# Kernel tuning notes

Measured on AMD Instinct MI355X. Metric: run time of the kernel, lower is better.

Reference implementation:

```python
import jax, jax.numpy as jnp
import numpy as np

B, L, N, HID, NH, HD, SH, SW, MH = 1, 512, 2048, 2048, 16, 128, 64, 32, 8192


def _rms(x, w, eps=1e-6):
    return x * jax.lax.rsqrt(jnp.mean(x * x, axis=-1, keepdims=True) + eps) * w


def _adaln(x, emb, W, b, nw):
    e = jax.nn.silu(emb) @ W + b  # [B, 6*hid]
    sh_m, sc_m, g_m, sh_p, sc_p, g_p = jnp.split(e, 6, axis=-1)
    xm = _rms(x, nw) * (1.0 + sc_m[:, None]) + sh_m[:, None]
    return xm, g_m, sh_p, sc_p, g_p


def _rope(x, rope):
    # x: [B, H, S, D], rope: [S, 1, D]
    f = rope[:, 0]  # [S, D]
    cos = jnp.repeat(f[:, 0::2], 2, axis=-1)[None, None]
    sin = jnp.repeat(f[:, 1::2], 2, axis=-1)[None, None]
    xr = x.reshape(*x.shape[:-1], -1, 2)
    x_rot = jnp.stack([-xr[..., 1], xr[..., 0]], axis=-1).reshape(x.shape)
    return x * cos + x_rot * sin


def _sdpa(q, k, v, scale):
    s = jnp.einsum('bhqd,bhkd->bhqk', q, k) * scale
    return jnp.einsum('bhqk,bhkd->bhqd', jax.nn.softmax(s, axis=-1), v)


def _mlp(x, w1, b1, w2, b2):
    return jax.nn.gelu(x @ w1 + b1, approximate=True) @ w2 + b2


def setup_inputs() -> dict:
    key = jax.random.key(0)
    ks = iter(jax.random.split(key, 32))
    r = lambda *s: jax.random.normal(next(ks), s, dtype=jnp.float32) * 0.02
    inp = {
        'txt': jax.random.normal(next(ks), (B, L, HID), dtype=jnp.float32),
        'img': jax.random.normal(next(ks), (B, N, HID), dtype=jnp.float32),
        'vec': jax.random.normal(next(ks), (B, HID), dtype=jnp.float32),
        'rope': jax.random.normal(next(ks), (N, 1, HD), dtype=jnp.float32),
        'sol_temperature': jax.random.uniform(next(ks), (B, 64), dtype=jnp.float32),
        'sol_spatial': jax.random.normal(next(ks), (B, 8, 8), dtype=jnp.float32),
        'ada_img_w': r(HID, 6 * HID), 'ada_img_b': jnp.zeros(6 * HID, jnp.float32), 'ada_img_nw': jnp.ones(HID, jnp.float32),
        'ada_txt_w': r(HID, 6 * HID), 'ada_txt_b': jnp.zeros(6 * HID, jnp.float32), 'ada_txt_nw': jnp.ones(HID, jnp.float32),
        'txt_qkv_w': r(HID, 3 * HID), 'img_qkv_w': r(HID, 3 * HID),
        'txt_out_w': r(HID, HID), 'img_out_w': r(HID, HID),
        'mod_w': r(NH) * 5.0, 'mod_b': r(NH) * 5.0,
        'img_n2_w': jnp.ones(HID, jnp.float32), 'txt_n2_w': jnp.ones(HID, jnp.float32),
        'img_fc1_w': r(HID, MH), 'img_fc1_b': jnp.zeros(MH, jnp.float32),
        'img_fc2_w': r(MH, HID), 'img_fc2_b': jnp.zeros(HID, jnp.float32),
        'txt_fc1_w': r(HID, MH), 'txt_fc1_b': jnp.zeros(MH, jnp.float32),
        'txt_fc2_w': r(MH, HID), 'txt_fc2_b': jnp.zeros(HID, jnp.float32),
        'spatial_h': SH, 'spatial_w': SW,
    }
    return inp


def reference(txt, img, vec, rope, sol_temperature, sol_spatial,
              ada_img_w, ada_img_b, ada_img_nw, ada_txt_w, ada_txt_b, ada_txt_nw,
              txt_qkv_w, img_qkv_w, txt_out_w, img_out_w, mod_w, mod_b,
              img_n2_w, txt_n2_w, img_fc1_w, img_fc1_b, img_fc2_w, img_fc2_b,
              txt_fc1_w, txt_fc1_b, txt_fc2_w, txt_fc2_b, spatial_h, spatial_w):
    b, l, hid = txt.shape
    n = img.shape[1]
    nh = mod_w.shape[0]
    hd = hid // nh
    scale = hd ** (-0.5)

    img_n, img_g, img_shp, img_scp, img_gp = _adaln(img, vec, ada_img_w, ada_img_b, ada_img_nw)
    txt_n, txt_g, txt_shp, txt_scp, txt_gp = _adaln(txt, vec, ada_txt_w, ada_txt_b, ada_txt_nw)

    def qkv(x, w, s):
        p = (x @ w).reshape(b, s, 3, nh, hd).transpose(2, 0, 3, 1, 4)  # [3,B,H,S,D]
        return p[0], p[1], p[2]

    tq, tk, tv = qkv(txt_n, txt_qkv_w, l)
    iq, ik, iv = qkv(img_n, img_qkv_w, n)
    iq = _rope(iq, rope)
    ik = _rope(ik, rope)

    # SOL spatial modulation: bilinear upsample (align_corners=False) + 1x1 conv + exp(clamp)
    sol_up = jax.image.resize(sol_spatial, (b, spatial_h, spatial_w), 'bilinear')
    mod = sol_up[:, None] * mod_w[None, :, None, None] + mod_b[None, :, None, None]
    mod = jnp.exp(jnp.clip(mod, -2.0, 2.0)).reshape(b, nh, n, 1)
    iq = iq * mod
    ik = ik * mod

    k = jnp.concatenate([tk, ik], axis=2)  # [B,H,L+N,D]
    v = jnp.concatenate([tv, iv], axis=2)

    txt_attn = _sdpa(tq, k, v, scale).transpose(0, 2, 1, 3).reshape(b, l, hid) @ txt_out_w

    temp = jnp.clip(jnp.mean(sol_temperature, axis=1, keepdims=True), 0.1)  # [B,1]
    s_eff = jnp.sqrt(scale / temp)[:, :, None, None]  # [B,1,1,1]
    img_attn = _sdpa(iq * s_eff, k * s_eff, v, 1.0).transpose(0, 2, 1, 3).reshape(b, n, hid) @ img_out_w

    txt = txt + txt_g[:, None] * txt_attn
    img = img + img_g[:, None] * img_attn

    txt_in = _rms(txt, txt_n2_w) * (1.0 + txt_scp[:, None]) + txt_shp[:, None]
    img_in = _rms(img, img_n2_w) * (1.0 + img_scp[:, None]) + img_shp[:, None]
    txt = txt + txt_gp[:, None] * _mlp(txt_in, txt_fc1_w, txt_fc1_b, txt_fc2_w, txt_fc2_b)
    img = img + img_gp[:, None] * _mlp(img_in, img_fc1_w, img_fc1_b, img_fc2_w, img_fc2_b)
    return txt, img
```

## Files before the change

### kernel.cpp

```cpp
#include <hip/hip_runtime.h>

typedef short short8 __attribute__((ext_vector_type(8)));
typedef float f32x4 __attribute__((ext_vector_type(4)));

__device__ __forceinline__ unsigned short f2bu(float f) {
  unsigned u = __builtin_bit_cast(unsigned, f);
  u += 0x7fffu + ((u >> 16) & 1u);
  return (unsigned short)(u >> 16);
}

__device__ __forceinline__ unsigned short f2bt(float f) {
  return (unsigned short)(__builtin_bit_cast(unsigned, f) >> 16);
}

__device__ __forceinline__ float b2f(unsigned short b) {
  unsigned u = (unsigned)b << 16;
  return __builtin_bit_cast(float, u);
}

__device__ __forceinline__ float gelu_t(float x) {
  float x3 = x * x * x;
  float t = tanhf(0.7978845608028654f * (x + 0.044715f * x3));
  return 0.5f * x * (1.f + t);
}

__device__ __forceinline__ void gload16(const void* g, void* l) {
  __builtin_amdgcn_global_load_lds(
      (const __attribute__((address_space(1))) void*)g,
      (__attribute__((address_space(3))) void*)l, 16, 0, 0);
}

__global__ __launch_bounds__(256) void prep_small(
    const float* __restrict__ vec, const float* __restrict__ sol_t,
    float* __restrict__ silu_vec, float* __restrict__ scales) {
  __shared__ float red[4];
  int t = threadIdx.x;
  float v = (t < 64) ? sol_t[t] : 0.f;
#pragma unroll
  for (int o = 32; o > 0; o >>= 1) v += __shfl_down(v, o);
  if ((t & 63) == 0) red[t >> 6] = v;
  __syncthreads();
  if (t == 0) {
    float m = (red[0] + red[1] + red[2] + red[3]) * (1.f / 64.f);
    m = fmaxf(m, 0.1f);
    const float sc = 0.08838834764831845f;
    const float l2e = 1.4426950408889634f;
    scales[0] = sc * l2e;
    scales[1] = sc / m * l2e;
  }
  for (int k = t; k < 2048; k += 256) {
    float x = vec[k];
    silu_vec[k] = x / (1.f + expf(-x));
  }
}

__global__ __launch_bounds__(256) void mod_kernel(
    const float* __restrict__ S, const float* __restrict__ mw,
    const float* __restrict__ mb, float* __restrict__ modb) {
  int idx = blockIdx.x * 256 + threadIdx.x;
  int h = idx >> 11, n = idx & 2047;
  int y = n >> 5, x = n & 31;
  float cy = (y + 0.5f) * 0.125f - 0.5f;
  float cx = (x + 0.5f) * 0.25f - 0.5f;
  int y0 = (int)floorf(cy); float fy = cy - (float)y0;
  int x0 = (int)floorf(cx); float fx = cx - (float)x0;
  int y0c = min(max(y0, 0), 7), y1c = min(max(y0 + 1, 0), 7);
  int x0c = min(max(x0, 0), 7), x1c = min(max(x0 + 1, 0), 7);
  float v = (1.f - fy) * ((1.f - fx) * S[y0c * 8 + x0c] + fx * S[y0c * 8 + x1c]) +
            fy * ((1.f - fx) * S[y1c * 8 + x0c] + fx * S[y1c * 8 + x1c]);
  float t = v * mw[h] + mb[h];
  t = fminf(fmaxf(t, -2.f), 2.f);
  modb[idx] = expf(t);
}

__global__ __launch_bounds__(256) void ada_gemv(
    const float* __restrict__ sv,
    const float* __restrict__ Wi, const float* __restrict__ bi,
    const float* __restrict__ Wt, const float* __restrict__ bt,
    float* __restrict__ ei, float* __restrict__ et) {
  __shared__ float red[4][64];
  const float* W = blockIdx.y ? Wt : Wi;
  const float* bb = blockIdx.y ? bt : bi;
  float* e = blockIdx.y ? et : ei;
  int jl = threadIdx.x & 63, ks = threadIdx.x >> 6;
  int j = blockIdx.x * 64 + jl;
  float acc = 0.f;
  int k0 = ks * 512;
#pragma unroll 4
  for (int k = 0; k < 512; ++k) acc += sv[k0 + k] * W[(size_t)(k0 + k) * 12288 + j];
  red[ks][jl] = acc;
  __syncthreads();
  if (ks == 0) e[j] = red[0][jl] + red[1][jl] + red[2][jl] + red[3][jl] + bb[j];
}

__global__ __launch_bounds__(256) void norm1_kernel(
    const float* __restrict__ txt, const float* __restrict__ img,
    const float* __restrict__ nw_t, const float* __restrict__ nw_i,
    const float* __restrict__ e_t, const float* __restrict__ e_i,
    unsigned short* __restrict__ out) {
  __shared__ float red[4];
  int r = blockIdx.x, t = threadIdx.x;
  bool ist = r < 512;
  const float* X = ist ? txt + (size_t)r * 2048 : img + (size_t)(r - 512) * 2048;
  const float* nw = ist ? nw_t : nw_i;
  const float* e = ist ? e_t : e_i;
  const float4* xr = reinterpret_cast<const float4*>(X);
  float4 v0 = xr[t * 2], v1 = xr[t * 2 + 1];
  float ss = v0.x * v0.x + v0.y * v0.y + v0.z * v0.z + v0.w * v0.w +
             v1.x * v1.x + v1.y * v1.y + v1.z * v1.z + v1.w * v1.w;
#pragma unroll
  for (int o = 32; o > 0; o >>= 1) ss += __shfl_down(ss, o);
  if ((t & 63) == 0) red[t >> 6] = ss;
  __syncthreads();
  float rinv = rsqrtf((red[0] + red[1] + red[2] + red[3]) * (1.f / 2048.f) + 1e-6f);
  int c0 = t * 8;
  float xv[8] = {v0.x, v0.y, v0.z, v0.w, v1.x, v1.y, v1.z, v1.w};
  short8 ov;
#pragma unroll
  for (int i = 0; i < 8; ++i) {
    int c = c0 + i;
    float y = xv[i] * rinv * nw[c] * (1.f + e[2048 + c]) + e[c];
    ov[i] = (short)f2bu(y);
  }
  *reinterpret_cast<short8*>(out + (size_t)r * 2048 + c0) = ov;
}

__global__ __launch_bounds__(256) void res1_rms(
    const float* __restrict__ txt, const float* __restrict__ img,
    const float* __restrict__ P0, const float* __restrict__ P1,
    const float* __restrict__ e_t, const float* __restrict__ e_i,
    const float* __restrict__ nw_t, const float* __restrict__ nw_i,
    float* __restrict__ out, unsigned short* __restrict__ actA) {
  __shared__ float red[4];
  int r = blockIdx.x, t = threadIdx.x;
  bool ist = r < 512;
  const float* X = ist ? txt + (size_t)r * 2048 : img + (size_t)(r - 512) * 2048;
  const float* e = ist ? e_t : e_i;
  const float* nw = ist ? nw_t : nw_i;
  int c0 = t * 8;
  const float* p0 = P0 + (size_t)r * 2048 + c0;
  const float* p1 = P1 + (size_t)r * 2048 + c0;
  float o[8];
  float ss = 0.f;
#pragma unroll
  for (int i = 0; i < 8; i += 4) {
    float4 x = *reinterpret_cast<const float4*>(X + c0 + i);
    float4 a = *reinterpret_cast<const float4*>(p0 + i);
    float4 b = *reinterpret_cast<const float4*>(p1 + i);
    float4 g = *reinterpret_cast<const float4*>(e + 4096 + c0 + i);
    o[i + 0] = x.x + g.x * (a.x + b.x);
    o[i + 1] = x.y + g.y * (a.y + b.y);
    o[i + 2] = x.z + g.z * (a.z + b.z);
    o[i + 3] = x.w + g.w * (a.w + b.w);
    ss += o[i] * o[i] + o[i + 1] * o[i + 1] + o[i + 2] * o[i + 2] + o[i + 3] * o[i + 3];
  }
  *reinterpret_cast<float4*>(out + (size_t)r * 2048 + c0) =
      make_float4(o[0], o[1], o[2], o[3]);
  *reinterpret_cast<float4*>(out + (size_t)r * 2048 + c0 + 4) =
      make_float4(o[4], o[5], o[6], o[7]);
#pragma unroll
  for (int of = 32; of > 0; of >>= 1) ss += __shfl_down(ss, of);
  if ((t & 63) == 0) red[t >> 6] = ss;
  __syncthreads();
  float rinv = rsqrtf((red[0] + red[1] + red[2] + red[3]) * (1.f / 2048.f) + 1e-6f);
  short8 ov;
#pragma unroll
  for (int i = 0; i < 8; ++i) {
    int c = c0 + i;
    float y = o[i] * rinv * nw[c] * (1.f + e[8192 + c]) + e[6144 + c];
    ov[i] = (short)f2bu(y);
  }
  *reinterpret_cast<short8*>(actA + (size_t)r * 2048 + c0) = ov;
}

__global__ __launch_bounds__(256) void res2_kernel(
    const float* __restrict__ P0, const float* __restrict__ P1,
    const float* __restrict__ b_t, const float* __restrict__ b_i,
    const float* __restrict__ e_t, const float* __restrict__ e_i,
    float* __restrict__ out) {
  int r = blockIdx.x, t = threadIdx.x;
  bool ist = r < 512;
  const float* e = ist ? e_t : e_i;
  const float* bb = ist ? b_t : b_i;
  int c0 = t * 8;
  const float* p0 = P0 + (size_t)r * 2048 + c0;
  const float* p1 = P1 + (size_t)r * 2048 + c0;
  float* op = out + (size_t)r * 2048 + c0;
#pragma unroll
  for (int i = 0; i < 8; i += 4) {
    float4 a = *reinterpret_cast<const float4*>(p0 + i);
    float4 b = *reinterpret_cast<const float4*>(p1 + i);
    float4 g = *reinterpret_cast<const float4*>(e + 10240 + c0 + i);
    float4 bv = *reinterpret_cast<const float4*>(bb + c0 + i);
    float4 o = *reinterpret_cast<const float4*>(op + i);
    o.x += g.x * (a.x + b.x + bv.x);
    o.y += g.y * (a.y + b.y + bv.y);
    o.z += g.z * (a.z + b.z + bv.z);
    o.w += g.w * (a.w + b.w + bv.w);
    *reinterpret_cast<float4*>(op + i) = o;
  }
}

__global__ __launch_bounds__(256) void transpose_w(
    const float* __restrict__ W, unsigned short* __restrict__ Bt, int K, int N) {
  __shared__ float tile[64][33];
  int n0 = blockIdx.x * 32, k0 = blockIdx.y * 64;
  int tid = threadIdx.x;
  int tx = tid & 31, ty = tid >> 5;
#pragma unroll
  for (int j = 0; j < 8; ++j)
    tile[ty + j * 8][tx] = W[(size_t)(k0 + ty + j * 8) * N + n0 + tx];
  __syncthreads();
  int n = tid >> 3, ks = (tid & 7) * 8;
  unsigned pk[4];
#pragma unroll
  for (int i = 0; i < 4; ++i) {
    float lo = tile[ks + 2 * i][n], hi = tile[ks + 2 * i + 1][n];
    pk[i] = (unsigned)f2bu(lo) | ((unsigned)f2bu(hi) << 16);
  }
  int4 ov = make_int4(pk[0], pk[1], pk[2], pk[3]);
  *reinterpret_cast<int4*>(Bt + (size_t)(n0 + n) * K + k0 + ks) = ov;
}

__global__ __launch_bounds__(256) void transpose_v(
    const unsigned short* __restrict__ V, unsigned short* __restrict__ Vt) {
  __shared__ unsigned short tile[32][33];
  int h = blockIdx.z;
  int s0 = blockIdx.x * 32, d0 = blockIdx.y * 32;
  int tx = threadIdx.x, ty = threadIdx.y;
  const unsigned short* src = V + (size_t)h * 2560 * 128;
  unsigned short* dst = Vt + (size_t)h * 128 * 2560;
#pragma unroll
  for (int j = 0; j < 32; j += 8)
    tile[ty + j][tx] = src[(size_t)(s0 + ty + j) * 128 + d0 + tx];
  __syncthreads();
#pragma unroll
  for (int j = 0; j < 32; j += 8)
    dst[(size_t)(d0 + ty + j) * 2560 + s0 + tx] = tile[tx][ty + j];
}

struct GemmP {
  const unsigned short *A, *Bt_t, *Bt_i;
  float* C;
  unsigned short* Cb;
  const float *bias_t, *bias_i;
  const float *rope, *modb;
  unsigned short *q_txt, *q_img, *k_cat, *v_cat;
  const float* scales;
  int Mb_t;
  int N, K, KS;
};

template <int EPI>
__global__ __launch_bounds__(256) void gemm2(GemmP p) {
  __shared__ __align__(16) char GRAW[65536];
  int4* sAb = reinterpret_cast<int4*>(GRAW);
  int4* sBb = reinterpret_cast<int4*>(GRAW + 32768);
  const int NB = gridDim.x, MBT = gridDim.y;
  int nwg = NB * MBT;
  int orig = blockIdx.y * NB + blockIdx.x;
  int qq = nwg >> 3, rr = nwg & 7, xcd = orig & 7, base = orig >> 3;
  int sw = (xcd < rr ? xcd * (qq + 1) : rr * (qq + 1) + (xcd - rr) * qq) + base;
  int bx = sw / MBT, by = sw % MBT;
  const bool is_t = by < p.Mb_t;
  const unsigned short* Bt = is_t ? p.Bt_t : p.Bt_i;
  const int m0 = by * 128, n0 = bx * 128;
  const int z = blockIdx.z;
  const int Kz = p.K / p.KS, kbeg = z * Kz, kend = kbeg + Kz;
  const int tid = threadIdx.x;
  const int w = tid >> 6, l = tid & 63, lr = l & 15, lg = l >> 4;
  const int wm = (w >> 1) * 64, wn = (w & 1) * 64;
  f32x4 acc[4][4] = {};
  const int4* Ag = reinterpret_cast<const int4*>(p.A);
  const int4* Bg = reinterpret_cast<const int4*>(Bt);
  const int K8 = p.K >> 3;
  int srow[4], sch[4];
#pragma unroll
  for (int i = 0; i < 4; ++i) {
    int s = i * 256 + tid;
    srow[i] = s >> 3;
    sch[i] = (s & 7) ^ (srow[i] & 7);
  }
  {
    int kc = kbeg >> 3;
#pragma unroll
    for (int i = 0; i < 4; ++i) {
      gload16(&Ag[(size_t)(m0 + srow[i]) * K8 + kc + sch[i]], &sAb[i * 256 + w * 64]);
      gload16(&Bg[(size_t)(n0 + srow[i]) * K8 + kc + sch[i]], &sBb[i * 256 + w * 64]);
    }
  }
  asm volatile("s_waitcnt vmcnt(0)" ::: "memory");
  __builtin_amdgcn_sched_barrier(0);
  __builtin_amdgcn_s_barrier();
  int cur = 0;
  for (int k0 = kbeg; k0 < kend; k0 += 64) {
    if (k0 + 64 < kend) {
      int kc = (k0 + 64) >> 3;
      int nb = (cur ^ 1) * 1024;
#pragma unroll
      for (int i = 0; i < 4; ++i) {
        gload16(&Ag[(size_t)(m0 + srow[i]) * K8 + kc + sch[i]], &sAb[nb + i * 256 + w * 64]);
        gload16(&Bg[(size_t)(n0 + srow[i]) * K8 + kc + sch[i]], &sBb[nb + i * 256 + w * 64]);
      }
      __builtin_amdgcn_sched_barrier(0);
    }
    const short8* pA = reinterpret_cast<const short8*>(sAb + cur * 1024);
    const short8* pB = reinterpret_cast<const short8*>(sBb + cur * 1024);
    __builtin_amdgcn_s_setprio(1);
#pragma unroll
    for (int kk = 0; kk < 2; ++kk) {
      short8 af[4], bf[4];
#pragma unroll
      for (int m = 0; m < 4; ++m) {
        int row = wm + m * 16 + lr;
        af[m] = pA[row * 8 + ((kk * 4 + lg) ^ (row & 7))];
      }
#pragma unroll
      for (int n = 0; n < 4; ++n) {
        int row = wn + n * 16 + lr;
        bf[n] = pB[row * 8 + ((kk * 4 + lg) ^ (row & 7))];
      }
#pragma unroll
      for (int m = 0; m < 4; ++m)
#pragma unroll
        for (int n = 0; n < 4; ++n)
          acc[m][n] = __builtin_amdgcn_mfma_f32_16x16x32_bf16(af[m], bf[n], acc[m][n], 0, 0, 0);
    }
    __builtin_amdgcn_s_setprio(0);
    asm volatile("s_waitcnt vmcnt(0)" ::: "memory");
    __builtin_amdgcn_sched_barrier(0);
    __builtin_amdgcn_s_barrier();
    cur ^= 1;
  }
  if (EPI == 0) {
    float* C = p.C + (size_t)z * MBT * 128 * p.N;
#pragma unroll
    for (int m = 0; m < 4; ++m)
#pragma unroll
      for (int n = 0; n < 4; ++n)
#pragma unroll
        for (int j = 0; j < 4; ++j) {
          int r = m0 + wm + m * 16 + lg * 4 + j;
          int cc = n0 + wn + n * 16 + lr;
          C[(size_t)r * p.N + cc] = acc[m][n][j];
        }
  } else if (EPI == 1) {
    const float* bias = is_t ? p.bias_t : p.bias_i;
#pragma unroll
    for (int n = 0; n < 4; ++n) {
      int cc = n0 + wn + n * 16 + lr;
      float bv = bias[cc];
#pragma unroll
      for (int m = 0; m < 4; ++m)
#pragma unroll
        for (int j = 0; j < 4; ++j) {
          int r = m0 + wm + m * 16 + lg * 4 + j;
          p.Cb[(size_t)r * p.N + cc] = f2bu(gelu_t(acc[m][n][j] + bv));
        }
    }
  } else {
    unsigned short* osh = reinterpret_cast<unsigned short*>(GRAW);
#pragma unroll
    for (int m = 0; m < 4; ++m)
#pragma unroll
      for (int n = 0; n < 4; ++n)
#pragma unroll
        for (int j = 0; j < 4; ++j) {
          int row = wm + m * 16 + lg * 4 + j;
          int col = wn + n * 16 + lr;
          osh[row * 136 + col] = f2bu(acc[m][n][j]);
        }
    __syncthreads();
    int sel = bx >> 4, h = bx & 15;
    int row = tid >> 1, d0 = (tid & 1) * 64;
    int r = m0 + row;
    const unsigned short* src = osh + row * 136 + d0;
    if (is_t) {
      if (sel == 0) {
        float qs = p.scales[0];
        unsigned short* dst = p.q_txt + ((size_t)h * 512 + r) * 128 + d0;
#pragma unroll
        for (int i = 0; i < 8; ++i) {
          short8 v = *reinterpret_cast<const short8*>(src + i * 8);
          short8 o;
#pragma unroll
          for (int t = 0; t < 8; ++t)
            o[t] = (short)f2bu(b2f((unsigned short)v[t]) * qs);
          *reinterpret_cast<short8*>(dst + i * 8) = o;
        }
      } else {
        unsigned short* dst =
            (sel == 1 ? p.k_cat : p.v_cat) + ((size_t)h * 2560 + r) * 128 + d0;
#pragma unroll
        for (int i = 0; i < 8; ++i)
          *reinterpret_cast<short8*>(dst + i * 8) =
              *reinterpret_cast<const short8*>(src + i * 8);
      }
    } else {
      int s = r - 512;
      if (sel == 2) {
        unsigned short* dst = p.v_cat + ((size_t)h * 2560 + r) * 128 + d0;
#pragma unroll
        for (int i = 0; i < 8; ++i)
          *reinterpret_cast<short8*>(dst + i * 8) =
              *reinterpret_cast<const short8*>(src + i * 8);
      } else {
        float mv = p.modb[h * 2048 + s];
        float qs = (sel == 0) ? p.scales[1] * mv : mv;
        const float2* rp = reinterpret_cast<const float2*>(p.rope + (size_t)s * 128 + d0);
        unsigned short* dst = (sel == 0)
            ? p.q_img + ((size_t)h * 2048 + s) * 128 + d0
            : p.k_cat + ((size_t)h * 2560 + r) * 128 + d0;
#pragma unroll
        for (int i = 0; i < 8; ++i) {
          short8 v = *reinterpret_cast<const short8*>(src + i * 8);
          short8 o;
#pragma unroll
          for (int t = 0; t < 4; ++t) {
            float2 cs = rp[i * 4 + t];
            float e = b2f((unsigned short)v[2 * t]);
            float od = b2f((unsigned short)v[2 * t + 1]);
            o[2 * t] = (short)f2bu((e * cs.x - od * cs.y) * qs);
            o[2 * t + 1] = (short)f2bu((od * cs.x + e * cs.y) * qs);
          }
          *reinterpret_cast<short8*>(dst + i * 8) = o;
        }
      }
    }
  }
}

__global__ __launch_bounds__(256, 4) void attn_kernel(
    const unsigned short* __restrict__ q_txt, const unsigned short* __restrict__ q_img,
    const unsigned short* __restrict__ Kc, const unsigned short* __restrict__ Vt,
    unsigned short* __restrict__ Op, float* __restrict__ ml) {
  __shared__ __align__(16) char RAW[40960];
  int4* sK = reinterpret_cast<int4*>(RAW);
  int4* sV = reinterpret_cast<int4*>(RAW + 16384);
  int4* sP = reinterpret_cast<int4*>(RAW + 32768);
  unsigned short* osh = reinterpret_cast<unsigned short*>(RAW);
  const int tid = threadIdx.x, w = tid >> 6, l = tid & 63, lr = l & 15, lg = l >> 4;
  int flat = blockIdx.x + 40 * (blockIdx.y + 16 * blockIdx.z);
  int sw = (flat & 7) * 320 + (flat >> 3);
  const int bx = sw % 40;
  int hz = sw / 40;
  const int h = hz & 15, z = hz >> 4;
  const bool is_t = bx < 8;
  const int orow = is_t ? bx * 64 : 512 + (bx - 8) * 64;
  const unsigned short* Qp = is_t ? q_txt + ((size_t)h * 512 + bx * 64) * 128
                                  : q_img + ((size_t)h * 2048 + (bx - 8) * 64) * 128;
  short8 aq[4];
#pragma unroll
  for (int ds = 0; ds < 4; ++ds) {
    int row = w * 16 + lr;
    aq[ds] = *reinterpret_cast<const short8*>(Qp + (size_t)row * 128 + ds * 32 + lg * 8);
  }
  const int4* Kg = reinterpret_cast<const int4*>(Kc + (size_t)h * 2560 * 128);
  const int4* Vg = reinterpret_cast<const int4*>(Vt + (size_t)h * 128 * 2560);
  const short8* pK = reinterpret_cast<const short8*>(sK);
  const short8* pV = reinterpret_cast<const short8*>(sV);
  const short8* pP = reinterpret_cast<const short8*>(sP);
  unsigned short* sPb = reinterpret_cast<unsigned short*>(sP);
  int krow[4], kch[4], vrow[4], vch[4];
#pragma unroll
  for (int i = 0; i < 4; ++i) {
    int s = i * 256 + tid;
    krow[i] = s >> 4; kch[i] = (s & 15) ^ (krow[i] & 7);
    vrow[i] = s >> 3; vch[i] = (s & 7) ^ (vrow[i] & 7);
  }
  short8 ones8;
#pragma unroll
  for (int i = 0; i < 8; ++i) ones8[i] = (short)0x3F80;

  f32x4 oacc[8] = {};
  f32x4 oacc_l = {};
  float m_run[4];
#pragma unroll
  for (int j = 0; j < 4; ++j) m_run[j] = -1e30f;

  const int kbeg = z * 10, kend = kbeg + 10;
#pragma unroll
  for (int i = 0; i < 4; ++i)
    gload16(&Kg[(size_t)(kbeg * 64 + krow[i]) * 16 + kch[i]], &sK[i * 256 + w * 64]);
#pragma unroll
  for (int i = 0; i < 4; ++i)
    gload16(&Vg[(size_t)vrow[i] * 320 + kbeg * 8 + vch[i]], &sV[i * 256 + w * 64]);

  for (int kt = kbeg; kt < kend; ++kt) {
    asm volatile("s_waitcnt vmcnt(4)" ::: "memory");
    __builtin_amdgcn_sched_barrier(0);
    __builtin_amdgcn_s_barrier();
    f32x4 sacc[4] = {};
    __builtin_amdgcn_s_setprio(1);
#pragma unroll
    for (int ds = 0; ds < 4; ++ds) {
      short8 bk[4];
#pragma unroll
      for (int n = 0; n < 4; ++n) {
        int row = n * 16 + lr;
        bk[n] = pK[row * 16 + ((ds * 4 + lg) ^ (row & 7))];
      }
#pragma unroll
      for (int n = 0; n < 4; ++n)
        sacc[n] = __builtin_amdgcn_mfma_f32_16x16x32_bf16(aq[ds], bk[n], sacc[n], 0, 0, 0);
    }
    __builtin_amdgcn_s_setprio(0);
    __builtin_amdgcn_s_barrier();
    if (kt + 1 < kend) {
#pragma unroll
      for (int i = 0; i < 4; ++i)
        gload16(&Kg[(size_t)((kt + 1) * 64 + krow[i]) * 16 + kch[i]], &sK[i * 256 + w * 64]);
    }
    float corr_[4];
    bool grow_any = false;
#pragma unroll
    for (int j = 0; j < 4; ++j) {
      float mx = fmaxf(fmaxf(sacc[0][j], sacc[1][j]), fmaxf(sacc[2][j], sacc[3][j]));
      mx = fmaxf(mx, __shfl_xor(mx, 1));
      mx = fmaxf(mx, __shfl_xor(mx, 2));
      mx = fmaxf(mx, __shfl_xor(mx, 4));
      mx = fmaxf(mx, __shfl_xor(mx, 8));
      bool grow = mx > m_run[j] + 11.0f;
      grow_any |= grow;
      float mn = grow ? mx : m_run[j];
      corr_[j] = grow ? exp2f(m_run[j] - mn) : 1.0f;
      m_run[j] = mn;
      int prow = w * 16 + lg * 4 + j;
#pragma unroll
      for (int n = 0; n < 4; ++n) {
        float pp = exp2f(sacc[n][j] - mn);
        int col = n * 16 + lr;
        sPb[prow * 64 + (((col >> 3) ^ (prow & 7)) << 3) + (col & 7)] = f2bt(pp);
      }
    }
    if (__any(grow_any)) {
#pragma unroll
      for (int n = 0; n < 8; ++n)
#pragma unroll
        for (int j = 0; j < 4; ++j) oacc[n][j] *= corr_[j];
#pragma unroll
      for (int j = 0; j < 4; ++j) oacc_l[j] *= corr_[j];
    }
    if (kt + 1 < kend) {
      asm volatile("s_waitcnt vmcnt(4)" ::: "memory");
    } else {
      asm volatile("s_waitcnt vmcnt(0)" ::: "memory");
    }
    __builtin_amdgcn_sched_barrier(0);
    __builtin_amdgcn_s_barrier();
    __builtin_amdgcn_s_setprio(1);
#pragma unroll
    for (int kk = 0; kk < 2; ++kk) {
      short8 ap, bv[8];
      {
        int row = w * 16 + lr;
        ap = pP[row * 8 + ((kk * 4 + lg) ^ (row & 7))];
      }
#pragma unroll
      for (int n = 0; n < 8; ++n) {
        int row = n * 16 + lr;
        bv[n] = pV[row * 8 + ((kk * 4 + lg) ^ (row & 7))];
      }
#pragma unroll
      for (int n = 0; n < 8; ++n)
        oacc[n] = __builtin_amdgcn_mfma_f32_16x16x32_bf16(ap, bv[n], oacc[n], 0, 0, 0);
      oacc_l = __builtin_amdgcn_mfma_f32_16x16x32_bf16(ap, ones8, oacc_l, 0, 0, 0);
    }
    __builtin_amdgcn_s_setprio(0);
    __builtin_amdgcn_s_barrier();
    if (kt + 1 < kend) {
#pragma unroll
      for (int i = 0; i < 4; ++i)
        gload16(&Vg[(size_t)vrow[i] * 320 + (kt + 1) * 8 + vch[i]], &sV[i * 256 + w * 64]);
    }
  }
  const size_t zbase = (size_t)z * 40960 + (size_t)h * 2560 + orow;
  __syncthreads();
#pragma unroll
  for (int j = 0; j < 4; ++j) {
    int row = w * 16 + lg * 4 + j;
#pragma unroll
    for (int n = 0; n < 8; ++n)
      osh[row * 136 + n * 16 + lr] = f2bt(oacc[n][j]);
    if (lr == 0) {
      ml[(zbase + row) * 2] = m_run[j];
      ml[(zbase + row) * 2 + 1] = oacc_l[j];
    }
  }
  __syncthreads();
  {
    int row = tid >> 2, c0 = (tid & 3) * 32;
#pragma unroll
    for (int i = 0; i < 4; ++i)
      *reinterpret_cast<short8*>(Op + (zbase + row) * 128 + c0 + i * 8) =
          *reinterpret_cast<const short8*>(osh + row * 136 + c0 + i * 8);
  }
}

__global__ __launch_bounds__(256) void attn_merge(
    const unsigned short* __restrict__ Op, const float* __restrict__ ml,
    unsigned short* __restrict__ ao) {
  int gid = blockIdx.x * 256 + threadIdx.x;
  int rid = gid >> 5, d0 = (gid & 31) * 4;
  int h = rid / 2560;
  int r = rid - h * 2560;
  float M = -1e30f;
#pragma unroll
  for (int z = 0; z < 4; ++z) M = fmaxf(M, ml[((size_t)z * 40960 + rid) * 2]);
  float L = 0.f, o0 = 0.f, o1 = 0.f, o2 = 0.f, o3 = 0.f;
#pragma unroll
  for (int z = 0; z < 4; ++z) {
    size_t sidx = (size_t)z * 40960 + rid;
    float mz = ml[sidx * 2], lz = ml[sidx * 2 + 1];
    float wgt = exp2f(mz - M);
    L += wgt * lz;
    ushort4 v = *reinterpret_cast<const ushort4*>(Op + sidx * 128 + d0);
    o0 += wgt * b2f(v.x); o1 += wgt * b2f(v.y);
    o2 += wgt * b2f(v.z); o3 += wgt * b2f(v.w);
  }
  float inv = 1.f / L;
  ushort4 ov;
  ov.x = f2bu(o0 * inv); ov.y = f2bu(o1 * inv);
  ov.z = f2bu(o2 * inv); ov.w = f2bu(o3 * inv);
  *reinterpret_cast<ushort4*>(ao + (size_t)r * 2048 + h * 128 + d0) = ov;
}

extern "C" void kernel_launch(void* const* d_in, const int* in_sizes, int n_in,
                              void* d_out, int out_size, void* d_ws, size_t ws_size,
                              hipStream_t stream) {
  (void)in_sizes; (void)n_in; (void)out_size; (void)ws_size;
  const float* txt = (const float*)d_in[0];
  const float* img = (const float*)d_in[1];
  const float* vec = (const float*)d_in[2];
  const float* rope = (const float*)d_in[3];
  const float* sol_t = (const float*)d_in[4];
  const float* sol_s = (const float*)d_in[5];
  const float* ada_img_w = (const float*)d_in[6];
  const float* ada_img_b = (const float*)d_in[7];
  const float* ada_img_nw = (const float*)d_in[8];
  const float* ada_txt_w = (const float*)d_in[9];
  const float* ada_txt_b = (const float*)d_in[10];
  const float* ada_txt_nw = (const float*)d_in[11];
  const float* txt_qkv_w = (const float*)d_in[12];
  const float* img_qkv_w = (const float*)d_in[13];
  const float* txt_out_w = (const float*)d_in[14];
  const float* img_out_w = (const float*)d_in[15];
  const float* mod_w = (const float*)d_in[16];
  const float* mod_b = (const float*)d_in[17];
  const float* img_n2_w = (const float*)d_in[18];
  const float* txt_n2_w = (const float*)d_in[19];
  const float* img_fc1_w = (const float*)d_in[20];
  const float* img_fc1_b = (const float*)d_in[21];
  const float* img_fc2_w = (const float*)d_in[22];
  const float* img_fc2_b = (const float*)d_in[23];
  const float* txt_fc1_w = (const float*)d_in[24];
  const float* txt_fc1_b = (const float*)d_in[25];
  const float* txt_fc2_w = (const float*)d_in[26];
  const float* txt_fc2_b = (const float*)d_in[27];
  float* out = (float*)d_out;
  char* ws = (char*)d_ws;

  const size_t MB = 1 << 20;
  float* silu_vec = (float*)(ws + 0);
  float* scales = (float*)(ws + 8192);
  float* modb = (float*)(ws + 16384);
  float* e_img = (float*)(ws + 147456);
  float* e_txt = (float*)(ws + 196608);
  unsigned short* wt0 = (unsigned short*)(ws + 1 * MB);
  unsigned short* wt1 = (unsigned short*)(ws + 33 * MB);
  unsigned short* Opart = (unsigned short*)(ws + 1 * MB);
  float* mlbuf = (float*)(ws + 42 * MB);
  unsigned short* actA = (unsigned short*)(ws + 65 * MB);
  char* attn_base = ws + 75 * MB;
  unsigned short* q_txt = (unsigned short*)(attn_base);
  unsigned short* q_img = (unsigned short*)(attn_base + 2 * MB);
  unsigned short* k_cat = (unsigned short*)(attn_base + 10 * MB);
  unsigned short* v_cat = (unsigned short*)(attn_base + 20 * MB);
  unsigned short* vT = (unsigned short*)(attn_base + 30 * MB);
  unsigned short* ao = (unsigned short*)(attn_base + 40 * MB);
  unsigned short* actB = (unsigned short*)attn_base;
  float* Cbuf = (float*)(ws + 125 * MB);
  const size_t PSTR = (size_t)2560 * 2048;

  prep_small<<<1, 256, 0, stream>>>(vec, sol_t, silu_vec, scales);
  mod_kernel<<<128, 256, 0, stream>>>(sol_s, mod_w, mod_b, modb);
  ada_gemv<<<dim3(192, 2), 256, 0, stream>>>(silu_vec, ada_img_w, ada_img_b,
                                             ada_txt_w, ada_txt_b, e_img, e_txt);
  norm1_kernel<<<2560, 256, 0, stream>>>(txt, img, ada_txt_nw, ada_img_nw,
                                         e_txt, e_img, actA);
  transpose_w<<<dim3(192, 32), 256, 0, stream>>>(txt_qkv_w, wt0, 2048, 6144);
  transpose_w<<<dim3(192, 32), 256, 0, stream>>>(img_qkv_w, wt1, 2048, 6144);
  {
    GemmP p = {actA, wt0, wt1, nullptr, nullptr, nullptr, nullptr,
               rope, modb, q_txt, q_img, k_cat, v_cat, scales, 4, 6144, 2048, 1};
    gemm2<2><<<dim3(48, 20, 1), 256, 0, stream>>>(p);
  }
  transpose_v<<<dim3(80, 4, 16), dim3(32, 8), 0, stream>>>(v_cat, vT);
  attn_kernel<<<dim3(40, 16, 4), 256, 0, stream>>>(q_txt, q_img, k_cat, vT, Opart, mlbuf);
  attn_merge<<<5120, 256, 0, stream>>>(Opart, mlbuf, ao);
  transpose_w<<<dim3(64, 32), 256, 0, stream>>>(txt_out_w, wt0, 2048, 2048);
  transpose_w<<<dim3(64, 32), 256, 0, stream>>>(img_out_w, wt1, 2048, 2048);
  {
    GemmP p = {ao, wt0, wt1, Cbuf, nullptr, nullptr, nullptr,
               nullptr, nullptr, nullptr, nullptr, nullptr, nullptr, nullptr, 4, 2048, 2048, 2};
    gemm2<0><<<dim3(16, 20, 2), 256, 0, stream>>>(p);
  }
  res1_rms<<<2560, 256, 0, stream>>>(txt, img, Cbuf, Cbuf + PSTR, e_txt, e_img,
                                     txt_n2_w, img_n2_w, out, actA);
  transpose_w<<<dim3(256, 32), 256, 0, stream>>>(txt_fc1_w, wt0, 2048, 8192);
  transpose_w<<<dim3(256, 32), 256, 0, stream>>>(img_fc1_w, wt1, 2048, 8192);
  {
    GemmP p = {actA, wt0, wt1, nullptr, actB, txt_fc1_b, img_fc1_b,
               nullptr, nullptr, nullptr, nullptr, nullptr, nullptr, nullptr, 4, 8192, 2048, 1};
    gemm2<1><<<dim3(64, 20, 1), 256, 0, stream>>>(p);
  }
  transpose_w<<<dim3(64, 128), 256, 0, stream>>>(txt_fc2_w, wt0, 8192, 2048);
  transpose_w<<<dim3(64, 128), 256, 0, stream>>>(img_fc2_w, wt1, 8192, 2048);
  {
    GemmP p = {actB, wt0, wt1, Cbuf, nullptr, nullptr, nullptr,
               nullptr, nullptr, nullptr, nullptr, nullptr, nullptr, nullptr, 4, 2048, 8192, 2};
    gemm2<0><<<dim3(16, 20, 2), 256, 0, stream>>>(p);
  }
  res2_kernel<<<2560, 256, 0, stream>>>(Cbuf, Cbuf + PSTR, txt_fc2_b, img_fc2_b,
                                        e_txt, e_img, out);
}
```

Baseline: 715.0 us.

## Drop split-K for out-proj and fc2 GEMMs and fuse final residual into epilogue

The out-projection and fc2 GEMMs drop from a split-K of 2 to a single K pass, so res1_rms reads one partial buffer instead of two. The fc2 GEMM gets a new epilogue that adds bias, applies the gate and accumulates into the output residual directly, which removes res2_kernel and its extra fp32 round trips. The cost is half as many workgroups (320 tiles) for these GEMMs, which may underfill the GPU, especially for the K=8192 fc2. The fused epilogue also rounds the accumulator to bf16 through shared memory before adding it, which loses precision.

```diff
diff --git a/kernel.cpp b/kernel.cpp
--- a/kernel.cpp
+++ b/kernel.cpp
@@ -127,7 +127,7 @@
 
 __global__ __launch_bounds__(256) void res1_rms(
     const float* __restrict__ txt, const float* __restrict__ img,
-    const float* __restrict__ P0, const float* __restrict__ P1,
+    const float* __restrict__ P0,
     const float* __restrict__ e_t, const float* __restrict__ e_i,
     const float* __restrict__ nw_t, const float* __restrict__ nw_i,
     float* __restrict__ out, unsigned short* __restrict__ actA) {
@@ -139,19 +139,17 @@
   const float* nw = ist ? nw_t : nw_i;
   int c0 = t * 8;
   const float* p0 = P0 + (size_t)r * 2048 + c0;
-  const float* p1 = P1 + (size_t)r * 2048 + c0;
   float o[8];
   float ss = 0.f;
 #pragma unroll
   for (int i = 0; i < 8; i += 4) {
     float4 x = *reinterpret_cast<const float4*>(X + c0 + i);
     float4 a = *reinterpret_cast<const float4*>(p0 + i);
-    float4 b = *reinterpret_cast<const float4*>(p1 + i);
     float4 g = *reinterpret_cast<const float4*>(e + 4096 + c0 + i);
-    o[i + 0] = x.x + g.x * (a.x + b.x);
-    o[i + 1] = x.y + g.y * (a.y + b.y);
-    o[i + 2] = x.z + g.z * (a.z + b.z);
-    o[i + 3] = x.w + g.w * (a.w + b.w);
+    o[i + 0] = x.x + g.x * a.x;
+    o[i + 1] = x.y + g.y * a.y;
+    o[i + 2] = x.z + g.z * a.z;
+    o[i + 3] = x.w + g.w * a.w;
     ss += o[i] * o[i] + o[i + 1] * o[i + 1] + o[i + 2] * o[i + 2] + o[i + 3] * o[i + 3];
   }
   *reinterpret_cast<float4*>(out + (size_t)r * 2048 + c0) =
@@ -171,34 +169,6 @@
     ov[i] = (short)f2bu(y);
   }
   *reinterpret_cast<short8*>(actA + (size_t)r * 2048 + c0) = ov;
-}
-
-__global__ __launch_bounds__(256) void res2_kernel(
-    const float* __restrict__ P0, const float* __restrict__ P1,
-    const float* __restrict__ b_t, const float* __restrict__ b_i,
-    const float* __restrict__ e_t, const float* __restrict__ e_i,
-    float* __restrict__ out) {
-  int r = blockIdx.x, t = threadIdx.x;
-  bool ist = r < 512;
-  const float* e = ist ? e_t : e_i;
-  const float* bb = ist ? b_t : b_i;
-  int c0 = t * 8;
-  const float* p0 = P0 + (size_t)r * 2048 + c0;
-  const float* p1 = P1 + (size_t)r * 2048 + c0;
-  float* op = out + (size_t)r * 2048 + c0;
-#pragma unroll
-  for (int i = 0; i < 8; i += 4) {
-    float4 a = *reinterpret_cast<const float4*>(p0 + i);
-    float4 b = *reinterpret_cast<const float4*>(p1 + i);
-    float4 g = *reinterpret_cast<const float4*>(e + 10240 + c0 + i);
-    float4 bv = *reinterpret_cast<const float4*>(bb + c0 + i);
-    float4 o = *reinterpret_cast<const float4*>(op + i);
-    o.x += g.x * (a.x + b.x + bv.x);
-    o.y += g.y * (a.y + b.y + bv.y);
-    o.z += g.z * (a.z + b.z + bv.z);
-    o.w += g.w * (a.w + b.w + bv.w);
-    *reinterpret_cast<float4*>(op + i) = o;
-  }
 }
 
 __global__ __launch_bounds__(256) void transpose_w(
@@ -247,6 +217,7 @@
   const float *rope, *modb;
   unsigned short *q_txt, *q_img, *k_cat, *v_cat;
   const float* scales;
+  const float *ga_t, *ga_i;
   int Mb_t;
   int N, K, KS;
 };
@@ -357,6 +328,36 @@
           int r = m0 + wm + m * 16 + lg * 4 + j;
           p.Cb[(size_t)r * p.N + cc] = f2bu(gelu_t(acc[m][n][j] + bv));
         }
+    }
+  } else if (EPI == 3) {
+    unsigned short* osh = reinterpret_cast<unsigned short*>(GRAW);
+#pragma unroll
+    for (int m = 0; m < 4; ++m)
+#pragma unroll
+      for (int n = 0; n < 4; ++n)
+#pragma unroll
+        for (int j = 0; j < 4; ++j) {
+          int row = wm + m * 16 + lg * 4 + j;
+          int col = wn + n * 16 + lr;
+          osh[row * 136 + col] = f2bu(acc[m][n][j]);
+        }
+    __syncthreads();
+    const float* gat = (is_t ? p.ga_t : p.ga_i) + 10240;
+    const float* bias = is_t ? p.bias_t : p.bias_i;
+    int row = tid >> 1, d0 = (tid & 1) * 64;
+    int r = m0 + row;
+    const unsigned short* src = osh + row * 136 + d0;
+    float* op = p.C + (size_t)r * p.N + n0 + d0;
+#pragma unroll
+    for (int i = 0; i < 16; ++i) {
+      float4 o = *reinterpret_cast<const float4*>(op + i * 4);
+      float4 g = *reinterpret_cast<const float4*>(gat + n0 + d0 + i * 4);
+      float4 bv = *reinterpret_cast<const float4*>(bias + n0 + d0 + i * 4);
+      o.x += g.x * (b2f(src[i * 4 + 0]) + bv.x);
+      o.y += g.y * (b2f(src[i * 4 + 1]) + bv.y);
+      o.z += g.z * (b2f(src[i * 4 + 2]) + bv.z);
+      o.w += g.w * (b2f(src[i * 4 + 3]) + bv.w);
+      *reinterpret_cast<float4*>(op + i * 4) = o;
     }
   } else {
     unsigned short* osh = reinterpret_cast<unsigned short*>(GRAW);
@@ -681,6 +682,7 @@
   unsigned short* actB = (unsigned short*)attn_base;
   float* Cbuf = (float*)(ws + 125 * MB);
   const size_t PSTR = (size_t)2560 * 2048;
+  (void)PSTR;
 
   prep_small<<<1, 256, 0, stream>>>(vec, sol_t, silu_vec, scales);
   mod_kernel<<<128, 256, 0, stream>>>(sol_s, mod_w, mod_b, modb);
@@ -692,7 +694,8 @@
   transpose_w<<<dim3(192, 32), 256, 0, stream>>>(img_qkv_w, wt1, 2048, 6144);
   {
     GemmP p = {actA, wt0, wt1, nullptr, nullptr, nullptr, nullptr,
-               rope, modb, q_txt, q_img, k_cat, v_cat, scales, 4, 6144, 2048, 1};
+               rope, modb, q_txt, q_img, k_cat, v_cat, scales,
+               nullptr, nullptr, 4, 6144, 2048, 1};
     gemm2<2><<<dim3(48, 20, 1), 256, 0, stream>>>(p);
   }
   transpose_v<<<dim3(80, 4, 16), dim3(32, 8), 0, stream>>>(v_cat, vT);
@@ -702,25 +705,26 @@
   transpose_w<<<dim3(64, 32), 256, 0, stream>>>(img_out_w, wt1, 2048, 2048);
   {
     GemmP p = {ao, wt0, wt1, Cbuf, nullptr, nullptr, nullptr,
-               nullptr, nullptr, nullptr, nullptr, nullptr, nullptr, nullptr, 4, 2048, 2048, 2};
-    gemm2<0><<<dim3(16, 20, 2), 256, 0, stream>>>(p);
-  }
-  res1_rms<<<2560, 256, 0, stream>>>(txt, img, Cbuf, Cbuf + PSTR, e_txt, e_img,
+               nullptr, nullptr, nullptr, nullptr, nullptr, nullptr, nullptr,
+               nullptr, nullptr, 4, 2048, 2048, 1};
+    gemm2<0><<<dim3(16, 20, 1), 256, 0, stream>>>(p);
+  }
+  res1_rms<<<2560, 256, 0, stream>>>(txt, img, Cbuf, e_txt, e_img,
                                      txt_n2_w, img_n2_w, out, actA);
   transpose_w<<<dim3(256, 32), 256, 0, stream>>>(txt_fc1_w, wt0, 2048, 8192);
   transpose_w<<<dim3(256, 32), 256, 0, stream>>>(img_fc1_w, wt1, 2048, 8192);
   {
     GemmP p = {actA, wt0, wt1, nullptr, actB, txt_fc1_b, img_fc1_b,
-               nullptr, nullptr, nullptr, nullptr, nullptr, nullptr, nullptr, 4, 8192, 2048, 1};
+               nullptr, nullptr, nullptr, nullptr, nullptr, nullptr, nullptr,
+               nullptr, nullptr, 4, 8192, 2048, 1};
     gemm2<1><<<dim3(64, 20, 1), 256, 0, stream>>>(p);
   }
   transpose_w<<<dim3(64, 128), 256, 0, stream>>>(txt_fc2_w, wt0, 8192, 2048);
   transpose_w<<<dim3(64, 128), 256, 0, stream>>>(img_fc2_w, wt1, 8192, 2048);
   {
-    GemmP p = {actB, wt0, wt1, Cbuf, nullptr, nullptr, nullptr,
-               nullptr, nullptr, nullptr, nullptr, nullptr, nullptr, nullptr, 4, 2048, 8192, 2};
-    gemm2<0><<<dim3(16, 20, 2), 256, 0, stream>>>(p);
-  }
-  res2_kernel<<<2560, 256, 0, stream>>>(Cbuf, Cbuf + PSTR, txt_fc2_b, img_fc2_b,
-                                        e_txt, e_img, out);
-}
+    GemmP p = {actB, wt0, wt1, out, nullptr, txt_fc2_b, img_fc2_b,
+               nullptr, nullptr, nullptr, nullptr, nullptr, nullptr, nullptr,
+               e_txt, e_img, 4, 2048, 8192, 1};
+    gemm2<3><<<dim3(16, 20, 1), 256, 0, stream>>>(p);
+  }
+}
```

Result: no change. 701.5 us (-1.9%).
